# Kernel tuning notes

Measured on AMD Instinct MI355X. Metric: run time of the kernel, lower is better.

The kernel has to match this reference:

```python
import jax, jax.numpy as jnp
import numpy as np

LN_EPS = 1e-5


def setup_inputs() -> dict:
    key = jax.random.key(0)
    k1, k2, k3, k4 = jax.random.split(key, 4)
    B, S, H, NH = 32, 256, 4096, 16
    scale = (2.0 ** 0.5) * ((3.0 / H) ** 0.5)
    inp = jax.random.normal(k1, (B, S, H), dtype=jnp.float32)
    mask = jax.random.randint(k2, (B, S), 0, 2, dtype=jnp.int32)  # 1 = padded key
    weight = jnp.ones((H,), dtype=jnp.float32)
    bias = jnp.zeros((H,), dtype=jnp.float32)
    qkv = jax.random.normal(k3, (H, 3 * H), dtype=jnp.float32) * scale
    o = jax.random.normal(k4, (H, H), dtype=jnp.float32) * scale
    return {"inp": inp, "mask": mask, "weight": weight, "bias": bias,
            "qkv": qkv, "o": o, "isPre": 1}


def _layer_norm(x, weight, bias):
    mu = jnp.mean(x, axis=-1, keepdims=True)
    var = jnp.mean(jnp.square(x - mu), axis=-1, keepdims=True)
    return (x - mu) * jax.lax.rsqrt(var + LN_EPS) * weight + bias


def _mha(x, mask, weight, bias, qkv, o, isPre, head_num=16):
    B, S, H = x.shape
    D = H // head_num
    xn = _layer_norm(x, weight, bias) if isPre else x
    # fused QKV projection: [B,S,3H]
    proj = jnp.einsum('bsh,hk->bsk', xn, qkv)
    q, k, v = jnp.split(proj, 3, axis=-1)
    q = q.reshape(B, S, head_num, D)
    k = k.reshape(B, S, head_num, D)
    v = v.reshape(B, S, head_num, D)
    scores = jnp.einsum('bqnd,bknd->bnqk', q, k) / jnp.sqrt(jnp.float32(D))
    # mask[b,k]==1 -> key k is padding, exclude from softmax
    neg = jnp.finfo(scores.dtype).min
    scores = jnp.where(mask[:, None, None, :] != 0, neg, scores)
    attn = jax.nn.softmax(scores, axis=-1)
    ctx = jnp.einsum('bnqk,bknd->bqnd', attn, v).reshape(B, S, H)
    out = jnp.einsum('bsh,ho->bso', ctx, o)
    if not isPre:
        out = _layer_norm(out, weight, bias)
    return out


def reference(inp, mask, weight, bias, qkv, o, isPre):
    return _mha(inp, mask, weight, bias, qkv, o, bool(isPre))
```

## Files before the change

### kernel.cpp

```cpp
#include <hip/hip_runtime.h>
#include <stdint.h>

typedef unsigned short u16;
typedef short bf16x8 __attribute__((ext_vector_type(8)));
typedef float f32x4 __attribute__((ext_vector_type(4)));
typedef unsigned short u16x8 __attribute__((ext_vector_type(8)));

#define MFMA16(a, b, c) __builtin_amdgcn_mfma_f32_16x16x32_bf16((a), (b), (c), 0, 0, 0)

#define GLOAD_LDS16(gp, lp)                                                        \
  __builtin_amdgcn_global_load_lds((const __attribute__((address_space(1))) void*)(gp), \
                                   (__attribute__((address_space(3))) void*)(lp), 16, 0, 0)

#define BARRIER asm volatile("s_barrier" ::: "memory")
#define WAITV(n) asm volatile("s_waitcnt vmcnt(" #n ")" ::: "memory")
#define WAITL0 asm volatile("s_waitcnt lgkmcnt(0)" ::: "memory")

__device__ __forceinline__ u16 f2bf(float x) {
  union { float f; uint32_t u; } v; v.f = x;
  uint32_t r = (v.u + 0x7FFFu + ((v.u >> 16) & 1u)) >> 16;
  return (u16)r;
}

__global__ __launch_bounds__(256) void transpose_bf16(const float* __restrict__ in,
                                                      u16* __restrict__ out, int R, int C) {
  __shared__ float tile[64][65];
  int nCt = C >> 6;
  int bid = blockIdx.x;
  int r0 = (bid / nCt) << 6, c0 = (bid % nCt) << 6;
  int t = threadIdx.x;
  int r = t >> 2, cg = (t & 3) << 4;
  const float* src = in + (size_t)(r0 + r) * C + c0 + cg;
#pragma unroll
  for (int i = 0; i < 4; i++) {
    float4 v = *reinterpret_cast<const float4*>(src + (i << 2));
    tile[r][cg + (i << 2) + 0] = v.x; tile[r][cg + (i << 2) + 1] = v.y;
    tile[r][cg + (i << 2) + 2] = v.z; tile[r][cg + (i << 2) + 3] = v.w;
  }
  __syncthreads();
  int c = t >> 2, rg = (t & 3) << 4;
  u16* dst = out + (size_t)(c0 + c) * R + r0 + rg;
#pragma unroll
  for (int i = 0; i < 2; i++) {
    u16x8 o8;
#pragma unroll
    for (int j2 = 0; j2 < 8; j2++) o8[j2] = f2bf(tile[rg + (i << 3) + j2][c]);
    *reinterpret_cast<u16x8*>(dst + (i << 3)) = o8;
  }
}

__global__ __launch_bounds__(256) void ln_bf16(const float* __restrict__ in,
                                               const float* __restrict__ w,
                                               const float* __restrict__ bia,
                                               u16* __restrict__ out) {
  int row = blockIdx.x, t = threadIdx.x;
  const float* x = in + (size_t)row * 4096;
  float4 v[4];
  float s = 0.f, sq = 0.f;
#pragma unroll
  for (int i = 0; i < 4; i++) {
    v[i] = *reinterpret_cast<const float4*>(x + i * 1024 + t * 4);
    s  += v[i].x + v[i].y + v[i].z + v[i].w;
    sq += v[i].x * v[i].x + v[i].y * v[i].y + v[i].z * v[i].z + v[i].w * v[i].w;
  }
#pragma unroll
  for (int off = 32; off > 0; off >>= 1) { s += __shfl_down(s, off); sq += __shfl_down(sq, off); }
  __shared__ float red[8];
  int wid = t >> 6, lane = t & 63;
  if (lane == 0) { red[wid] = s; red[4 + wid] = sq; }
  __syncthreads();
  if (t == 0) {
    float st = red[0] + red[1] + red[2] + red[3];
    float sqt = red[4] + red[5] + red[6] + red[7];
    float mu = st * (1.f / 4096.f);
    float var = sqt * (1.f / 4096.f) - mu * mu;
    red[0] = mu; red[1] = rsqrtf(var + 1e-5f);
  }
  __syncthreads();
  float mu = red[0], rs = red[1];
#pragma unroll
  for (int i = 0; i < 4; i++) {
    float4 wv = *reinterpret_cast<const float4*>(w + i * 1024 + t * 4);
    float4 bv = *reinterpret_cast<const float4*>(bia + i * 1024 + t * 4);
    ushort4 u;
    u.x = f2bf((v[i].x - mu) * rs * wv.x + bv.x);
    u.y = f2bf((v[i].y - mu) * rs * wv.y + bv.y);
    u.z = f2bf((v[i].z - mu) * rs * wv.z + bv.z);
    u.w = f2bf((v[i].w - mu) * rs * wv.w + bv.w);
    *reinterpret_cast<ushort4*>(out + (size_t)row * 4096 + i * 1024 + t * 4) = u;
  }
}


#define LDA8(AR, Ab, mh) do {                                                     \
  _Pragma("unroll")                                                               \
  for (int mf = 0; mf < 4; mf++) {                                                \
    int lr = (mh)*128 + wm64 + mf*16 + llo;                                       \
    const char* rb = (Ab) + lr*128;                                               \
    int sw = (lr & 7) << 4;                                                       \
    AR[mf*2+0] = *reinterpret_cast<const bf16x8*>(rb + ((lhi16) ^ sw));           \
    AR[mf*2+1] = *reinterpret_cast<const bf16x8*>(rb + ((64 + lhi16) ^ sw));      \
  }                                                                               \
} while (0)

#define LDB4(BR, Bb, nh) do {                                                     \
  _Pragma("unroll")                                                               \
  for (int nf = 0; nf < 2; nf++) {                                                \
    int lr = (nh)*128 + wn32 + nf*16 + llo;                                       \
    const char* rb = (Bb) + lr*128;                                               \
    int sw = (lr & 7) << 4;                                                       \
    BR[nf*2+0] = *reinterpret_cast<const bf16x8*>(rb + ((lhi16) ^ sw));           \
    BR[nf*2+1] = *reinterpret_cast<const bf16x8*>(rb + ((64 + lhi16) ^ sw));      \
  }                                                                               \
} while (0)

#define MMAQ(AR, BR, mh, nh) do {                                                 \
  _Pragma("unroll")                                                               \
  for (int mf = 0; mf < 4; mf++)                                                  \
    _Pragma("unroll")                                                             \
    for (int nf = 0; nf < 2; nf++) {                                              \
      acc[(mh)*4+mf][(nh)*2+nf] = MFMA16(AR[mf*2+0], BR[nf*2+0], acc[(mh)*4+mf][(nh)*2+nf]); \
      acc[(mh)*4+mf][(nh)*2+nf] = MFMA16(AR[mf*2+1], BR[nf*2+1], acc[(mh)*4+mf][(nh)*2+nf]); \
    }                                                                             \
} while (0)

#define STAGE(isB, h, cbuf, ktile) do {                                           \
  const u16* g_ = (isB) ? Bt : A;                                                 \
  int base0_ = (isB) ? n0 : m0;                                                   \
  char* lb_ = smc + (cbuf)*65536 + (isB)*32768 + (h)*16384;                       \
  _Pragma("unroll")                                                               \
  for (int i_ = 0; i_ < 2; i_++) {                                                \
    int L_ = i_*512 + t;                                                          \
    int lr_ = (h)*128 + (L_ >> 3);                                                \
    int sl_ = (L_ & 7) ^ (lr_ & 7);                                               \
    int r_ = (isB) ? (((lr_ & 128) >> 2) | ((lr_ & 96) << 1) | (lr_ & 31))        \
                   : ((lr_ & 63) | ((lr_ & 64) << 1) | ((lr_ & 128) >> 1));       \
    GLOAD_LDS16(g_ + (size_t)(base0_ + r_) * K + (ktile)*64 + sl_*8, lb_ + L_*16);\
  }                                                                               \
} while (0)

#define TILE2(tt, S1, S2, W2) do {                                                \
  int c_ = (tt) & 1;                                                              \
  const char* Ab = smc + c_ * 65536;                                              \
  const char* Bb = Ab + 32768;                                                    \
          \
  LDA8(aR, Ab, 0); LDB4(b0R, Bb, 0); LDB4(b1R, Bb, 1);                            \
  if (S1) { STAGE(1, 0, c_ ^ 1, (tt) + 1); STAGE(0, 1, c_ ^ 1, (tt) + 1); }       \
  __builtin_amdgcn_s_setprio(1);                                                  \
  MMAQ(aR, b0R, 0, 0); MMAQ(aR, b1R, 0, 1);                                       \
  __builtin_amdgcn_s_setprio(0);                                                  \
  WAITL0; BARRIER;                                                                \
                                     \
  LDA8(aR, Ab, 1);                                                                \
  if (S2) { STAGE(0, 0, c_, (tt) + 2); STAGE(1, 1, c_, (tt) + 2); }               \
  __builtin_amdgcn_s_setprio(1);                                                  \
  MMAQ(aR, b1R, 1, 1); MMAQ(aR, b0R, 1, 0);                                       \
  __builtin_amdgcn_s_setprio(0);                                                  \
  WAITV(W2); WAITL0; BARRIER;                                                     \
} while (0)

template <int EPI>
__global__ __launch_bounds__(512, 2) void gemm256(const u16* __restrict__ A, const u16* __restrict__ Bt,
                                                  void* __restrict__ Cout, u16* __restrict__ vT,
                                                  int M, int N, int K, int nbn) {
  __shared__ u16 sm[65536];
  char* smc = (char*)sm;
  int bid = blockIdx.x;
  int s = bid >> 8, local = bid & 255;
  int xcd = local & 7, j = local >> 3;
  int trow = ((xcd >> 1) << 2) + (j >> 3);
  int tcol = ((xcd & 1) << 3) + (j & 7);
  int nsc = nbn >> 4;
  int sr = s / nsc, sc = s - sr * nsc;
  int tm = (sr << 4) + trow, tn = (sc << 4) + tcol;
  int m0 = tm << 8, n0 = tn << 8;
  int t = threadIdx.x;
  int w = t >> 6, lane = t & 63;
  int wm = w >> 2, wn = w & 3;
  int llo = lane & 15, lhi = lane >> 4;
  int wm64 = wm << 6, wn32 = wn << 5, lhi16 = lhi << 4;
  f32x4 acc[8][4] = {};
  bf16x8 aR[8], b0R[4], b1R[4];
  int NT = K >> 6;
  STAGE(0, 0, 0, 0); STAGE(1, 0, 0, 0); STAGE(1, 1, 0, 0); STAGE(0, 1, 0, 0);
  STAGE(0, 0, 1, 1); STAGE(1, 1, 1, 1);
  WAITV(4); BARRIER;
#pragma unroll 1
  for (int tt = 0; tt < NT - 2; ++tt) TILE2(tt, 1, 1, 4);
  TILE2(NT - 2, 1, 0, 0);
  TILE2(NT - 1, 0, 0, 0);
  if (EPI == 2) {
    float* C = (float*)Cout;
#pragma unroll
    for (int mi = 0; mi < 8; mi++)
#pragma unroll
      for (int ni = 0; ni < 4; ni++) {
        int m = m0 + wm * 128 + mi * 16 + lhi * 4;
        int n = n0 + wn * 64 + ni * 16 + llo;
#pragma unroll
        for (int r = 0; r < 4; r++) C[(size_t)(m + r) * N + n] = acc[mi][ni][r];
      }
  } else {
    if (n0 < 8192) {
      u16* qkb = (u16*)Cout;
#pragma unroll
      for (int mi = 0; mi < 8; mi++)
#pragma unroll
        for (int ni = 0; ni < 4; ni++) {
          int m = m0 + wm * 128 + mi * 16 + lhi * 4;
          int n = n0 + wn * 64 + ni * 16 + llo;
#pragma unroll
          for (int r = 0; r < 4; r++) qkb[(size_t)(m + r) * 8192 + n] = f2bf(acc[mi][ni][r]);
        }
    } else {
#pragma unroll
      for (int mi = 0; mi < 8; mi++)
#pragma unroll
        for (int ni = 0; ni < 4; ni++) {
          int m = m0 + wm * 128 + mi * 16 + lhi * 4;
          int n_ = n0 + wn * 64 + ni * 16 + llo - 8192;
          int h = n_ >> 8, d = n_ & 255;
          int b = m >> 8, s2 = m & 255;
          ushort4 u;
          u.x = f2bf(acc[mi][ni][0]); u.y = f2bf(acc[mi][ni][1]);
          u.z = f2bf(acc[mi][ni][2]); u.w = f2bf(acc[mi][ni][3]);
          *reinterpret_cast<ushort4*>(vT + ((size_t)((b << 4) + h) * 256 + d) * 256 + s2) = u;
        }
    }
  }
}

__global__ __launch_bounds__(256) void attn_kernel(const u16* __restrict__ qk,
                                                   const u16* __restrict__ vT,
                                                   const int* __restrict__ mask,
                                                   u16* __restrict__ ctx) {
  __shared__ u16 P[64 * 256];
  int bid = blockIdx.x;
  int xcd = bid & 7, idx = bid >> 3;
  int qt = idx & 3;
  int bh = (xcd << 6) + (idx >> 2);
  int b = bh >> 4, h = bh & 15;
  int t = threadIdx.x, wid = t >> 6, lane = t & 63, llo = lane & 15, lhi = lane >> 4;
  bf16x8 qf[8];
  {
    const u16* qrow = qk + (size_t)((b << 8) + (qt << 6) + (wid << 4) + llo) * 8192 + (h << 8);
#pragma unroll
    for (int c = 0; c < 8; c++)
      qf[c] = *reinterpret_cast<const bf16x8*>(qrow + (lhi << 3) + (c << 5));
  }
  f32x4 sacc[16] = {};
  const u16* kbase = qk + (size_t)(b << 8) * 8192 + 4096 + (h << 8) + (lhi << 3);
#pragma unroll 1
  for (int kt = 0; kt < 4; kt++) {
#pragma unroll
    for (int nf = 0; nf < 4; nf++) {
      const u16* krow = kbase + (size_t)((kt << 6) + (nf << 4) + llo) * 8192;
#pragma unroll
      for (int c = 0; c < 8; c++) {
        bf16x8 kf = *reinterpret_cast<const bf16x8*>(krow + (c << 5));
        sacc[kt * 4 + nf] = MFMA16(qf[c], kf, sacc[kt * 4 + nf]);
      }
    }
  }
  float madd[16];
#pragma unroll
  for (int f = 0; f < 16; f++) {
    int key = ((f >> 2) << 6) + ((f & 3) << 4) + llo;
    madd[f] = mask[(b << 8) + key] ? -1e30f : 0.0f;
  }
  float mx[4] = {-3e38f, -3e38f, -3e38f, -3e38f};
#pragma unroll
  for (int f = 0; f < 16; f++)
#pragma unroll
    for (int r = 0; r < 4; r++) {
      float sv = sacc[f][r] * 0.0625f + madd[f];
      sacc[f][r] = sv;
      mx[r] = fmaxf(mx[r], sv);
    }
#pragma unroll
  for (int r = 0; r < 4; r++)
#pragma unroll
    for (int d = 1; d < 16; d <<= 1) mx[r] = fmaxf(mx[r], __shfl_xor(mx[r], d));
  float sum[4] = {0.f, 0.f, 0.f, 0.f};
#pragma unroll
  for (int f = 0; f < 16; f++)
#pragma unroll
    for (int r = 0; r < 4; r++) {
      float p = __expf(sacc[f][r] - mx[r]);
      sacc[f][r] = p;
      sum[r] += p;
    }
#pragma unroll
  for (int r = 0; r < 4; r++)
#pragma unroll
    for (int d = 1; d < 16; d <<= 1) sum[r] += __shfl_xor(sum[r], d);
  float rin[4];
#pragma unroll
  for (int r = 0; r < 4; r++) rin[r] = 1.f / sum[r];
#pragma unroll
  for (int r = 0; r < 4; r++) {
    int q = (wid << 4) + (lhi << 2) + r;
    char* pb = (char*)P + (q << 9);
    int sw = (q & 7) << 4;
#pragma unroll
    for (int f = 0; f < 16; f++) {
      int key = ((f >> 2) << 6) + ((f & 3) << 4) + llo;
      *reinterpret_cast<u16*>(pb + ((key << 1) ^ sw)) = f2bf(sacc[f][r] * rin[r]);
    }
  }
  WAITL0;
  f32x4 cacc[16] = {};
  const u16* vbase = vT + (size_t)bh * 65536 + (lhi << 3);
#pragma unroll 1
  for (int kt = 0; kt < 4; kt++) {
    bf16x8 pf[2];
    {
      int q = (wid << 4) + llo;
      const char* pb = (const char*)P + (q << 9);
      int sw = (q & 7) << 4;
#pragma unroll
      for (int c = 0; c < 2; c++)
        pf[c] = *reinterpret_cast<const bf16x8*>(pb + (((kt << 7) + (c << 6) + (lhi << 4)) ^ sw));
    }
#pragma unroll
    for (int mf = 0; mf < 16; mf++) {
      const u16* vrow = vbase + (size_t)((mf << 4) + llo) * 256 + (kt << 6);
#pragma unroll
      for (int c = 0; c < 2; c++) {
        bf16x8 vf = *reinterpret_cast<const bf16x8*>(vrow + (c << 5));
        cacc[mf] = MFMA16(vf, pf[c], cacc[mf]);
      }
    }
  }
  int token = (b << 8) + (qt << 6) + (wid << 4) + llo;
  u16* crow = ctx + (size_t)token * 4096 + (h << 8);
#pragma unroll
  for (int mf = 0; mf < 16; mf++) {
    ushort4 u;
    u.x = f2bf(cacc[mf][0]); u.y = f2bf(cacc[mf][1]);
    u.z = f2bf(cacc[mf][2]); u.w = f2bf(cacc[mf][3]);
    *reinterpret_cast<ushort4*>(crow + (mf << 4) + (lhi << 2)) = u;
  }
}

extern "C" void kernel_launch(void* const* d_in, const int* in_sizes, int n_in,
                              void* d_out, int out_size, void* d_ws, size_t ws_size,
                              hipStream_t stream) {
  const float* inp  = (const float*)d_in[0];
  const int*   mask = (const int*)d_in[1];
  const float* w    = (const float*)d_in[2];
  const float* bia  = (const float*)d_in[3];
  const float* qkvw = (const float*)d_in[4];
  const float* ow   = (const float*)d_in[5];
  const size_t MB = 1024ull * 1024ull;
  if (ws_size < 352 * MB) return;
  char* ws = (char*)d_ws;
  u16* xn   = (u16*)(ws);
  u16* qkvT = (u16*)(ws + 64 * MB);
  u16* qk   = (u16*)(ws + 160 * MB);
  u16* vT   = (u16*)(ws + 288 * MB);
  u16* oT   = (u16*)(ws + 64 * MB);
  u16* ctx  = (u16*)(ws);
  float* out = (float*)d_out;

  transpose_bf16<<<12288, 256, 0, stream>>>(qkvw, qkvT, 4096, 12288);
  ln_bf16<<<8192, 256, 0, stream>>>(inp, w, bia, xn);
  gemm256<1><<<1536, 512, 0, stream>>>(xn, qkvT, (void*)qk, vT, 8192, 12288, 4096, 48);
  transpose_bf16<<<4096, 256, 0, stream>>>(ow, oT, 4096, 4096);
  attn_kernel<<<2048, 256, 0, stream>>>(qk, vT, mask, ctx);
  gemm256<2><<<512, 512, 0, stream>>>(ctx, oT, (void*)out, nullptr, 8192, 4096, 4096, 16);
}
```

Before: 1.424 ms.

## Stage K/V tiles through double-buffered LDS in attention, 128 queries per block

```diff
diff --git a/kernel.cpp b/kernel.cpp
--- a/kernel.cpp
+++ b/kernel.cpp
@@ -230,44 +230,72 @@
   }
 }
 
-__global__ __launch_bounds__(256) void attn_kernel(const u16* __restrict__ qk,
+__global__ __launch_bounds__(512) void attn_kernel(const u16* __restrict__ qk,
                                                    const u16* __restrict__ vT,
                                                    const int* __restrict__ mask,
                                                    u16* __restrict__ ctx) {
-  __shared__ u16 P[64 * 256];
+  __shared__ u16 KV[2 * 32 * 1024 / 2];
+  __shared__ u16 P[128 * 256];
+  __shared__ float maskf[256];
+  char* kv0 = (char*)KV;
   int bid = blockIdx.x;
-  int xcd = bid & 7, idx = bid >> 3;
-  int qt = idx & 3;
-  int bh = (xcd << 6) + (idx >> 2);
-  int b = bh >> 4, h = bh & 15;
+  int half = bid & 1, h = (bid >> 1) & 15, b = bid >> 5;
+  int bh = (b << 4) + h;
   int t = threadIdx.x, wid = t >> 6, lane = t & 63, llo = lane & 15, lhi = lane >> 4;
+  if (t < 256) maskf[t] = mask[(b << 8) + t] ? -1e30f : 0.0f;
   bf16x8 qf[8];
   {
-    const u16* qrow = qk + (size_t)((b << 8) + (qt << 6) + (wid << 4) + llo) * 8192 + (h << 8);
+    const u16* qrow = qk + (size_t)((b << 8) + (half << 7) + (wid << 4) + llo) * 8192 + (h << 8);
 #pragma unroll
     for (int c = 0; c < 8; c++)
       qf[c] = *reinterpret_cast<const bf16x8*>(qrow + (lhi << 3) + (c << 5));
   }
+#define STAGE_K(kt, buf) do {                                                      \
+    char* lb_ = kv0 + (buf) * 32768;                                               \
+    _Pragma("unroll")                                                              \
+    for (int i_ = 0; i_ < 4; i_++) {                                               \
+      int G_ = (i_ << 9) + t;                                                      \
+      int key_ = G_ >> 5, g_ = G_ & 31;                                            \
+      int gs_ = g_ ^ (key_ & 7);                                                   \
+      const u16* src_ = qk + (size_t)((b << 8) + ((kt) << 6) + key_) * 8192 + 4096 \
+                        + (h << 8) + (gs_ << 3);                                   \
+      GLOAD_LDS16(src_, lb_ + (G_ << 4));                                          \
+    }                                                                              \
+  } while (0)
+#define STAGE_V(j, buf) do {                                                       \
+    char* lb_ = kv0 + (buf) * 32768;                                               \
+    _Pragma("unroll")                                                              \
+    for (int i_ = 0; i_ < 4; i_++) {                                               \
+      int G_ = (i_ << 9) + t;                                                      \
+      int d_ = G_ >> 3, g_ = G_ & 7;                                               \
+      int gs_ = g_ ^ (d_ & 7);                                                     \
+      const u16* src_ = vT + ((size_t)bh * 256 + d_) * 256 + ((j) << 6) + (gs_ << 3); \
+      GLOAD_LDS16(src_, lb_ + (G_ << 4));                                          \
+    }                                                                              \
+  } while (0)
   f32x4 sacc[16] = {};
-  const u16* kbase = qk + (size_t)(b << 8) * 8192 + 4096 + (h << 8) + (lhi << 3);
+  STAGE_K(0, 0);
 #pragma unroll 1
   for (int kt = 0; kt < 4; kt++) {
+    if (kt < 3) STAGE_K(kt + 1, (kt + 1) & 1); else STAGE_V(0, 0);
+    WAITV(4); BARRIER;
+    const char* kb0 = kv0 + (kt & 1) * 32768;
 #pragma unroll
     for (int nf = 0; nf < 4; nf++) {
-      const u16* krow = kbase + (size_t)((kt << 6) + (nf << 4) + llo) * 8192;
+      int kl = (nf << 4) + llo;
+      const char* kb = kb0 + (kl << 9);
+      int sw = (kl & 7) << 4;
 #pragma unroll
       for (int c = 0; c < 8; c++) {
-        bf16x8 kf = *reinterpret_cast<const bf16x8*>(krow + (c << 5));
+        bf16x8 kf = *reinterpret_cast<const bf16x8*>(kb + (((lhi << 4) + (c << 6)) ^ sw));
         sacc[kt * 4 + nf] = MFMA16(qf[c], kf, sacc[kt * 4 + nf]);
       }
     }
+    WAITL0; BARRIER;
   }
   float madd[16];
 #pragma unroll
-  for (int f = 0; f < 16; f++) {
-    int key = ((f >> 2) << 6) + ((f & 3) << 4) + llo;
-    madd[f] = mask[(b << 8) + key] ? -1e30f : 0.0f;
-  }
+  for (int f = 0; f < 16; f++) madd[f] = maskf[(f << 4) + llo];
   float mx[4] = {-3e38f, -3e38f, -3e38f, -3e38f};
 #pragma unroll
   for (int f = 0; f < 16; f++)
@@ -304,15 +332,17 @@
     int sw = (q & 7) << 4;
 #pragma unroll
     for (int f = 0; f < 16; f++) {
-      int key = ((f >> 2) << 6) + ((f & 3) << 4) + llo;
+      int key = (f << 4) + llo;
       *reinterpret_cast<u16*>(pb + ((key << 1) ^ sw)) = f2bf(sacc[f][r] * rin[r]);
     }
   }
   WAITL0;
   f32x4 cacc[16] = {};
-  const u16* vbase = vT + (size_t)bh * 65536 + (lhi << 3);
 #pragma unroll 1
-  for (int kt = 0; kt < 4; kt++) {
+  for (int j = 0; j < 4; j++) {
+    if (j < 3) { STAGE_V(j + 1, (j + 1) & 1); WAITV(4); } else { WAITV(0); }
+    BARRIER;
+    const char* vb0 = kv0 + (j & 1) * 32768;
     bf16x8 pf[2];
     {
       int q = (wid << 4) + llo;
@@ -320,19 +350,24 @@
       int sw = (q & 7) << 4;
 #pragma unroll
       for (int c = 0; c < 2; c++)
-        pf[c] = *reinterpret_cast<const bf16x8*>(pb + (((kt << 7) + (c << 6) + (lhi << 4)) ^ sw));
+        pf[c] = *reinterpret_cast<const bf16x8*>(pb + (((j << 7) + (c << 6) + (lhi << 4)) ^ sw));
     }
 #pragma unroll
     for (int mf = 0; mf < 16; mf++) {
-      const u16* vrow = vbase + (size_t)((mf << 4) + llo) * 256 + (kt << 6);
+      int dl = (mf << 4) + llo;
+      const char* vb = vb0 + (dl << 7);
+      int sw = (dl & 7) << 4;
 #pragma unroll
       for (int c = 0; c < 2; c++) {
-        bf16x8 vf = *reinterpret_cast<const bf16x8*>(vrow + (c << 5));
+        bf16x8 vf = *reinterpret_cast<const bf16x8*>(vb + (((lhi << 4) + (c << 6)) ^ sw));
         cacc[mf] = MFMA16(vf, pf[c], cacc[mf]);
       }
     }
-  }
-  int token = (b << 8) + (qt << 6) + (wid << 4) + llo;
+    if (j < 3) { WAITL0; BARRIER; }
+  }
+#undef STAGE_K
+#undef STAGE_V
+  int token = (b << 8) + (half << 7) + (wid << 4) + llo;
   u16* crow = ctx + (size_t)token * 4096 + (h << 8);
 #pragma unroll
   for (int mf = 0; mf < 16; mf++) {
@@ -367,6 +402,6 @@
   ln_bf16<<<8192, 256, 0, stream>>>(inp, w, bia, xn);
   gemm256<1><<<1536, 512, 0, stream>>>(xn, qkvT, (void*)qk, vT, 8192, 12288, 4096, 48);
   transpose_bf16<<<4096, 256, 0, stream>>>(ow, oT, 4096, 4096);
-  attn_kernel<<<2048, 256, 0, stream>>>(qk, vT, mask, ctx);
+  attn_kernel<<<1024, 512, 0, stream>>>(qk, vT, mask, ctx);
   gemm256<2><<<512, 512, 0, stream>>>(ctx, oT, (void*)out, nullptr, 8192, 4096, 4096, 16);
 }
```

Result: faster. 1.239 ms (-13.0%).
